# Performance work log

Hardware: AMD Instinct MI355X
Metric: run time of the kernel (lower is better)

## Reference

```python
import jax, jax.numpy as jnp
import numpy as np

B, DIN, DH, DOUT, E, GIN, GH = 16384, 480, 512, 360, 8, 64, 128


def setup_inputs() -> dict:
    key = jax.random.key(0)
    ks = jax.random.split(key, 16)

    def glorot(k, shape):
        bound = np.sqrt(6.0 / np.prod(shape[-2:]))
        return jax.random.uniform(k, shape, jnp.float32, -bound, bound)

    return {
        "x": jax.random.normal(ks[0], (B, DIN), jnp.float32),
        # norm stats: row0 = mean, row1 = std (kept away from 0)
        "Xnorm": jnp.stack([jax.random.normal(ks[1], (DIN,)) * 0.1,
                            jax.random.uniform(ks[2], (DIN,), minval=0.5, maxval=1.5)]),
        "Ynorm": jnp.stack([jax.random.normal(ks[3], (DOUT,)) * 0.1,
                            jax.random.uniform(ks[4], (DOUT,), minval=0.5, maxval=1.5)]),
        "G1_W": glorot(ks[5], (GIN, GH)), "G1_b": jnp.zeros((GH,), jnp.float32),
        "G2_W": glorot(ks[6], (GH, GH)), "G2_b": jnp.zeros((GH,), jnp.float32),
        "G3_W": glorot(ks[7], (GH, E)),  "G3_b": jnp.zeros((E,), jnp.float32),
        "W1": glorot(ks[8], (E, DIN, DH)), "b1": jnp.zeros((E, DH), jnp.float32),
        "W2": glorot(ks[9], (E, DH, DH)),  "b2": jnp.zeros((E, DH), jnp.float32),
        "W3": glorot(ks[10], (E, DH, DOUT)), "b3": jnp.zeros((E, DOUT), jnp.float32),
        "gating_indices": jnp.arange(GIN, dtype=jnp.int32),
    }


def expert_linear(h, w, W, b):
    # h: [B, I], w: [B, E], W: [E, I, O], b: [E, O]
    # sum_e w[:,e] * (h @ W[e] + b[e])
    y = jnp.einsum('bi,eio->beo', h, W)        # [B, E, O]
    return jnp.einsum('be,beo->bo', w, y) + w @ b


def reference(x, Xnorm, Ynorm, G1_W, G1_b, G2_W, G2_b, G3_W, G3_b,
              W1, b1, W2, b2, W3, b3, gating_indices):
    xn = (x - Xnorm[0]) / Xnorm[1]
    # gating network (dropout inactive at eval)
    g = xn[:, gating_indices]
    g = jax.nn.elu(g @ G1_W + G1_b)
    g = jax.nn.elu(g @ G2_W + G2_b)
    w = jax.nn.softmax(g @ G3_W + G3_b, axis=1)   # [B, E]
    # expert-blended main network
    m = jax.nn.elu(expert_linear(xn, w, W1, b1))
    m = jax.nn.elu(expert_linear(m, w, W2, b2))
    m = expert_linear(m, w, W3, b3)
    return m * Ynorm[1] + Ynorm[0]
```

## Files before the change

kernel.cpp:

```cpp
#include <hip/hip_runtime.h>
#include <hip/hip_bf16.h>
#include <math.h>

#define BATCH 16384
#define DIN   480
#define DH    512
#define DOUT  360
#define NEXP  8
#define GIN   64
#define GH    128
#define KP    512

typedef short bf16x8 __attribute__((ext_vector_type(8)));
typedef float f32x4  __attribute__((ext_vector_type(4)));

__device__ __forceinline__ short f2bf(float f) {
    __hip_bfloat16 h = __float2bfloat16(f);
    return *reinterpret_cast<short*>(&h);
}
__device__ __forceinline__ float eluf(float x) { return x > 0.f ? x : expf(x) - 1.f; }

__device__ __forceinline__ void gll16(const void* g, void* l) {
    __builtin_amdgcn_global_load_lds(
        (const __attribute__((address_space(1))) unsigned int*)g,
        (__attribute__((address_space(3))) unsigned int*)l, 16, 0, 0);
}

__global__ void prep_xn_kernel(const float* __restrict__ x,
                               const float* __restrict__ Xnorm,
                               short* __restrict__ xnbf) {
    const int tid = blockIdx.x * 256 + threadIdx.x;
    const int row = tid >> 6;
    const int c   = (tid & 63) * 8;
    short v8[8];
    if (c < DIN) {
        #pragma unroll
        for (int j = 0; j < 8; ++j) {
            float v = (x[(size_t)row * DIN + c + j] - Xnorm[c + j]) / Xnorm[DIN + c + j];
            v8[j] = f2bf(v);
        }
    } else {
        #pragma unroll
        for (int j = 0; j < 8; ++j) v8[j] = 0;
    }
    *(uint4*)&xnbf[(size_t)row * KP + c] = *(uint4*)v8;
}

__global__ void transpose_w_kernel(const float* __restrict__ src,
                                   short* __restrict__ dst,
                                   int K, int N, int NPAD) {
    __shared__ float tile[32][33];
    const int ntn = NPAD / 32;
    const int ntk = KP / 32;
    int lin = blockIdx.x;
    const int e  = lin / (ntk * ntn);
    lin -= e * ntk * ntn;
    const int kt = lin / ntn;
    const int nt = lin % ntn;
    const int t = threadIdx.x;
    #pragma unroll
    for (int r = 0; r < 4; ++r) {
        int idx = t + r * 256;
        int i = idx >> 5;
        int j = idx & 31;
        int k = kt * 32 + i;
        int n = nt * 32 + j;
        float v = (n < N && k < K) ? src[((size_t)e * K + k) * N + n] : 0.f;
        tile[i][j] = v;
    }
    __syncthreads();
    #pragma unroll
    for (int r = 0; r < 4; ++r) {
        int idx = t + r * 256;
        int i2 = idx & 31;
        int j2 = idx >> 5;
        dst[((size_t)e * NPAD + nt * 32 + j2) * KP + kt * 32 + i2] = f2bf(tile[i2][j2]);
    }
}

__global__ __launch_bounds__(256) void gating_kernel(
    const float* __restrict__ x, const float* __restrict__ Xnorm,
    const float* __restrict__ G1W, const float* __restrict__ G1b,
    const float* __restrict__ G2W, const float* __restrict__ G2b,
    const float* __restrict__ G3W, const float* __restrict__ G3b,
    const int* __restrict__ gidx, float* __restrict__ wout) {

    __shared__ float g2s[GH * GH];
    __shared__ float g3s[GH * NEXP];
    __shared__ float b1s[GH], b2s[GH], b3s[NEXP];
    __shared__ float g0b[4][GIN], h1b[4][GH], h2b[4][GH];

    const int t = threadIdx.x;
    const int lane = t & 63;
    const int wid  = t >> 6;

    for (int i = t; i < GH * GH; i += 256) g2s[i] = G2W[i];
    for (int i = t; i < GH * NEXP; i += 256) g3s[i] = G3W[i];
    if (t < GH) { b1s[t] = G1b[t]; b2s[t] = G2b[t]; }
    if (t < NEXP) b3s[t] = G3b[t];
    __syncthreads();

    const int gi = gidx[lane];
    const float mu = Xnorm[gi];
    const float inv_sig = 1.f / Xnorm[DIN + gi];

    for (int it = 0; it < 16; ++it) {
        const int row = (blockIdx.x * 4 + wid) * 16 + it;
        float g0 = (x[(size_t)row * DIN + gi] - mu) * inv_sig;
        g0b[wid][lane] = g0;
        __syncthreads();
        float h1a = b1s[lane], h1c = b1s[lane + 64];
        #pragma unroll 8
        for (int i = 0; i < GIN; ++i) {
            float g = g0b[wid][i];
            h1a += g * G1W[i * GH + lane];
            h1c += g * G1W[i * GH + lane + 64];
        }
        h1b[wid][lane] = eluf(h1a);
        h1b[wid][lane + 64] = eluf(h1c);
        __syncthreads();
        float h2a = b2s[lane], h2c = b2s[lane + 64];
        #pragma unroll 8
        for (int i = 0; i < GH; ++i) {
            float h = h1b[wid][i];
            h2a += h * g2s[i * GH + lane];
            h2c += h * g2s[i * GH + lane + 64];
        }
        h2b[wid][lane] = eluf(h2a);
        h2b[wid][lane + 64] = eluf(h2c);
        __syncthreads();
        const int e  = lane & 7;
        const int ch = lane >> 3;
        float p = 0.f;
        #pragma unroll
        for (int i2 = 0; i2 < 16; ++i2) {
            int i = ch * 16 + i2;
            p += h2b[wid][i] * g3s[i * NEXP + e];
        }
        p += __shfl_xor(p, 8);
        p += __shfl_xor(p, 16);
        p += __shfl_xor(p, 32);
        p += b3s[e];
        float mx = p;
        mx = fmaxf(mx, __shfl_xor(mx, 1));
        mx = fmaxf(mx, __shfl_xor(mx, 2));
        mx = fmaxf(mx, __shfl_xor(mx, 4));
        float ex = expf(p - mx);
        float sm = ex;
        sm += __shfl_xor(sm, 1);
        sm += __shfl_xor(sm, 2);
        sm += __shfl_xor(sm, 4);
        float wv = ex / sm;
        if (lane < NEXP) wout[(size_t)row * NEXP + lane] = wv;
        __syncthreads();
    }
}

template<int NPAD, int NREAL, int MODE>
__global__ __launch_bounds__(256, 2) void expert_v4_kernel(
    const short* __restrict__ A, const short* __restrict__ Wt,
    const float* __restrict__ wgate, const float* __restrict__ bias,
    const float* __restrict__ Ynorm, void* __restrict__ Out) {

    __shared__ __align__(16) short bufA[2][128 * 64];
    __shared__ __align__(16) short bufB[2][128 * 64];
    __shared__ float wlsT[NEXP][128];

    const int t = threadIdx.x;
    const int lane = t & 63;
    const int wid  = t >> 6;
    const int wr = wid >> 1, wc = wid & 1;
    const int l4 = lane >> 4, lr = lane & 15;

    constexpr int NN = NPAD / 128;
    const int nwg = 128 * NN;
    const int cpx = nwg >> 3;
    const int lb  = (blockIdx.x & 7) * cpx + (blockIdx.x >> 3);
    const int m0  = (lb / NN) * 128;
    const int n0  = (lb % NN) * 128;

    for (int i = t; i < NEXP * 128; i += 256) {
        int e = i >> 7, r = i & 127;
        wlsT[e][r] = wgate[(size_t)(m0 + r) * NEXP + e];
    }

    const int srow  = lane >> 3;
    const int sslot = (lane & 7) ^ srow;

    const short* baseA[4];
    const short* baseB[4];
    short* dstA[2][4];
    short* dstB[2][4];
    #pragma unroll
    for (int i = 0; i < 4; ++i) {
        int q = wid * 4 + i;
        baseA[i] = A  + (size_t)(m0 + q * 8 + srow) * KP + sslot * 8;
        baseB[i] = Wt + (size_t)(n0 + q * 8 + srow) * KP + sslot * 8;
        #pragma unroll
        for (int d = 0; d < 2; ++d) {
            dstA[d][i] = &bufA[d][q * 512];
            dstB[d][i] = &bufB[d][q * 512];
        }
    }

    f32x4 acc[4][4], accF[4][4];
    #pragma unroll
    for (int mi = 0; mi < 4; ++mi)
        #pragma unroll
        for (int ni = 0; ni < 4; ++ni) {
            acc[mi][ni]  = (f32x4){0.f, 0.f, 0.f, 0.f};
            accF[mi][ni] = (f32x4){0.f, 0.f, 0.f, 0.f};
        }

    #pragma unroll
    for (int i = 0; i < 4; ++i) {
        gll16(baseA[i], dstA[0][i]);
        gll16(baseB[i], dstB[0][i]);
    }
    __syncthreads();

    for (int s = 0; s < 8 * NEXP; ++s) {
        const int cur = s & 1;

        if (s < 8 * NEXP - 1) {
            const int sn  = s + 1;
            const int en  = sn >> 3;
            const int ktn = sn & 7;
            const size_t oa = (size_t)ktn * 64;
            const size_t ob = (size_t)en * NPAD * KP + (size_t)ktn * 64;
            #pragma unroll
            for (int i = 0; i < 4; ++i) gll16(baseA[i] + oa, dstA[cur ^ 1][i]);
            #pragma unroll
            for (int i = 0; i < 4; ++i) gll16(baseB[i] + ob, dstB[cur ^ 1][i]);
            asm volatile("s_waitcnt vmcnt(8)" ::: "memory");
        } else {
            asm volatile("s_waitcnt vmcnt(0)" ::: "memory");
        }
        asm volatile("s_barrier" ::: "memory");

        {
            const short* Ab = &bufA[cur][0];
            const short* Bb = &bufB[cur][0];
            #pragma unroll
            for (int kk = 0; kk < 2; ++kk) {
                const int xo = (kk * 32 + l4 * 8) ^ ((lr & 7) << 3);
                bf16x8 a[4], b[4];
                #pragma unroll
                for (int mi = 0; mi < 4; ++mi)
                    a[mi] = *(const bf16x8*)(Ab + (wr * 64 + mi * 16 + lr) * 64 + xo);
                #pragma unroll
                for (int ni = 0; ni < 4; ++ni)
                    b[ni] = *(const bf16x8*)(Bb + (wc * 64 + ni * 16 + lr) * 64 + xo);
                #pragma unroll
                for (int mi = 0; mi < 4; ++mi)
                    #pragma unroll
                    for (int ni = 0; ni < 4; ++ni)
                        acc[mi][ni] = __builtin_amdgcn_mfma_f32_16x16x32_bf16(
                            a[mi], b[ni], acc[mi][ni], 0, 0, 0);
            }
        }

        if ((s & 7) == 7) {
            const int e = s >> 3;
            #pragma unroll
            for (int mi = 0; mi < 4; ++mi) {
                f32x4 wv = *(const f32x4*)&wlsT[e][wr * 64 + mi * 16 + l4 * 4];
                #pragma unroll
                for (int ni = 0; ni < 4; ++ni) {
                    #pragma unroll
                    for (int j = 0; j < 4; ++j)
                        accF[mi][ni][j] += wv[j] * acc[mi][ni][j];
                    acc[mi][ni] = (f32x4){0.f, 0.f, 0.f, 0.f};
                }
            }
        }

        asm volatile("s_barrier" ::: "memory");
    }

    {
        float bv[4][NEXP];
        #pragma unroll
        for (int ni = 0; ni < 4; ++ni) {
            int ng = n0 + wc * 64 + ni * 16 + lr;
            #pragma unroll
            for (int e = 0; e < NEXP; ++e)
                bv[ni][e] = (ng < NREAL) ? bias[(size_t)e * NREAL + ng] : 0.f;
        }
        #pragma unroll
        for (int mi = 0; mi < 4; ++mi) {
            f32x4 wv[NEXP];
            #pragma unroll
            for (int e = 0; e < NEXP; ++e)
                wv[e] = *(const f32x4*)&wlsT[e][wr * 64 + mi * 16 + l4 * 4];
            #pragma unroll
            for (int ni = 0; ni < 4; ++ni)
                #pragma unroll
                for (int j = 0; j < 4; ++j) {
                    float sum = 0.f;
                    #pragma unroll
                    for (int e = 0; e < NEXP; ++e) sum += wv[e][j] * bv[ni][e];
                    accF[mi][ni][j] += sum;
                }
        }
    }

    #pragma unroll
    for (int mi = 0; mi < 4; ++mi) {
        #pragma unroll
        for (int j = 0; j < 4; ++j) {
            size_t rg = (size_t)(m0 + wr * 64 + mi * 16 + l4 * 4 + j);
            #pragma unroll
            for (int ni = 0; ni < 4; ++ni) {
                int ng = n0 + wc * 64 + ni * 16 + lr;
                float v = accF[mi][ni][j];
                if (MODE == 0) {
                    v = v > 0.f ? v : expf(v) - 1.f;
                    ((short*)Out)[rg * NPAD + ng] = f2bf(v);
                } else {
                    if (ng < NREAL)
                        ((float*)Out)[rg * NREAL + ng] = v * Ynorm[NREAL + ng] + Ynorm[ng];
                }
            }
        }
    }
}

extern "C" void kernel_launch(void* const* d_in, const int* in_sizes, int n_in,
                              void* d_out, int out_size, void* d_ws, size_t ws_size,
                              hipStream_t stream) {
    const float* x     = (const float*)d_in[0];
    const float* Xnorm = (const float*)d_in[1];
    const float* Ynorm = (const float*)d_in[2];
    const float* G1W   = (const float*)d_in[3];
    const float* G1b   = (const float*)d_in[4];
    const float* G2W   = (const float*)d_in[5];
    const float* G2b   = (const float*)d_in[6];
    const float* G3W   = (const float*)d_in[7];
    const float* G3b   = (const float*)d_in[8];
    const float* W1    = (const float*)d_in[9];
    const float* b1    = (const float*)d_in[10];
    const float* W2    = (const float*)d_in[11];
    const float* b2    = (const float*)d_in[12];
    const float* W3    = (const float*)d_in[13];
    const float* b3    = (const float*)d_in[14];
    const int*   gidx  = (const int*)d_in[15];

    char* ws = (char*)d_ws;
    size_t off = 0;
    short* xnbf = (short*)(ws + off); off += (size_t)BATCH * KP * 2;
    short* m1   = (short*)(ws + off); off += (size_t)BATCH * DH * 2;
    short* Wt1  = (short*)(ws + off); off += (size_t)NEXP * DH  * KP * 2;
    short* Wt2  = (short*)(ws + off); off += (size_t)NEXP * DH  * KP * 2;
    short* Wt3  = (short*)(ws + off); off += (size_t)NEXP * 384 * KP * 2;
    float* wg   = (float*)(ws + off); off += (size_t)BATCH * NEXP * 4;
    short* m2   = xnbf;
    if (off > ws_size) return;

    prep_xn_kernel<<<BATCH * 64 / 256, 256, 0, stream>>>(x, Xnorm, xnbf);

    transpose_w_kernel<<<NEXP * (KP / 32) * (DH / 32), 256, 0, stream>>>(W1, Wt1, DIN, DH, DH);
    transpose_w_kernel<<<NEXP * (KP / 32) * (DH / 32), 256, 0, stream>>>(W2, Wt2, DH, DH, DH);
    transpose_w_kernel<<<NEXP * (KP / 32) * (384 / 32), 256, 0, stream>>>(W3, Wt3, DH, DOUT, 384);

    gating_kernel<<<256, 256, 0, stream>>>(x, Xnorm, G1W, G1b, G2W, G2b, G3W, G3b, gidx, wg);

    expert_v4_kernel<DH, DH, 0>
        <<<(BATCH / 128) * (DH / 128), 256, 0, stream>>>(xnbf, Wt1, wg, b1, Ynorm, m1);
    expert_v4_kernel<DH, DH, 0>
        <<<(BATCH / 128) * (DH / 128), 256, 0, stream>>>(m1, Wt2, wg, b2, Ynorm, m2);
    expert_v4_kernel<384, DOUT, 1>
        <<<(BATCH / 128) * (384 / 128), 256, 0, stream>>>(m2, Wt3, wg, b3, Ynorm, (void*)d_out);
}
```

Baseline: 338.9 us.

## Restructure expert GEMM to load all experts per K-tile and reuse A fragments

```diff
diff --git a/kernel.cpp b/kernel.cpp
--- a/kernel.cpp
+++ b/kernel.cpp
@@ -157,149 +157,160 @@
 }
 
 template<int NPAD, int NREAL, int MODE>
-__global__ __launch_bounds__(256, 2) void expert_v4_kernel(
+__global__ __launch_bounds__(512, 1) void expert_v13_kernel(
     const short* __restrict__ A, const short* __restrict__ Wt,
     const float* __restrict__ wgate, const float* __restrict__ bias,
     const float* __restrict__ Ynorm, void* __restrict__ Out) {
 
-    __shared__ __align__(16) short bufA[2][128 * 64];
-    __shared__ __align__(16) short bufB[2][128 * 64];
-    __shared__ float wlsT[NEXP][128];
+    __shared__ __align__(16) short bufA[128 * 64];
+    __shared__ __align__(16) short bufB[NEXP][128 * 64];
+    __shared__ float    wlsT[NEXP][128];
+    __shared__ unsigned wpk2[512];
 
     const int t = threadIdx.x;
     const int lane = t & 63;
     const int wid  = t >> 6;
-    const int wr = wid >> 1, wc = wid & 1;
+    const int wr = wid >> 2;
+    const int wc = wid & 3;
     const int l4 = lane >> 4, lr = lane & 15;
 
     constexpr int NN = NPAD / 128;
-    const int nwg = 128 * NN;
-    const int cpx = nwg >> 3;
+    constexpr int nwg = (BATCH / 128) * NN;
+    constexpr int cpx = nwg / 8;
     const int lb  = (blockIdx.x & 7) * cpx + (blockIdx.x >> 3);
     const int m0  = (lb / NN) * 128;
     const int n0  = (lb % NN) * 128;
 
-    for (int i = t; i < NEXP * 128; i += 256) {
+    for (int i = t; i < NEXP * 128; i += 512) {
         int e = i >> 7, r = i & 127;
         wlsT[e][r] = wgate[(size_t)(m0 + r) * NEXP + e];
     }
-
-    const int srow  = lane >> 3;
-    const int sslot = (lane & 7) ^ srow;
-
-    const short* baseA[4];
-    const short* baseB[4];
-    short* dstA[2][4];
-    short* dstB[2][4];
-    #pragma unroll
-    for (int i = 0; i < 4; ++i) {
-        int q = wid * 4 + i;
-        baseA[i] = A  + (size_t)(m0 + q * 8 + srow) * KP + sslot * 8;
-        baseB[i] = Wt + (size_t)(n0 + q * 8 + srow) * KP + sslot * 8;
-        #pragma unroll
-        for (int d = 0; d < 2; ++d) {
-            dstA[d][i] = &bufA[d][q * 512];
-            dstB[d][i] = &bufB[d][q * 512];
-        }
-    }
-
-    f32x4 acc[4][4], accF[4][4];
+    {
+        int e = t >> 6, wr_ = (t >> 5) & 1, l4_ = (t >> 3) & 3, q = t & 7;
+        int mi_ = q >> 1, p = q & 1;
+        int r = wr_ * 64 + mi_ * 16 + l4_ * 4 + p * 2;
+        unsigned short b0 = (unsigned short)f2bf(wgate[(size_t)(m0 + r) * NEXP + e]);
+        unsigned short b1 = (unsigned short)f2bf(wgate[(size_t)(m0 + r + 1) * NEXP + e]);
+        wpk2[t] = ((unsigned)b1 << 16) | b0;
+    }
+
+    const int c0 = wid * 128 + lane;
+    const int c1 = c0 + 64;
+    const int r0 = c0 >> 3, s0 = (c0 & 7) ^ (r0 & 7);
+    const int r1 = c1 >> 3, s1 = (c1 & 7) ^ (r1 & 7);
+
+    const short* srcA0 = A + (size_t)(m0 + r0) * KP + s0 * 8;
+    const short* srcA1 = A + (size_t)(m0 + r1) * KP + s1 * 8;
+    const short* srcB0 = Wt + (size_t)(n0 + r0) * KP + s0 * 8;
+    const short* srcB1 = Wt + (size_t)(n0 + r1) * KP + s1 * 8;
+    short* const dstA0 = &bufA[c0 * 8];
+    short* const dstA1 = &bufA[c1 * 8];
+
+    f32x4 acc[4][2], accF[4][2];
     #pragma unroll
     for (int mi = 0; mi < 4; ++mi)
         #pragma unroll
-        for (int ni = 0; ni < 4; ++ni) {
-            acc[mi][ni]  = (f32x4){0.f, 0.f, 0.f, 0.f};
+        for (int ni = 0; ni < 2; ++ni)
             accF[mi][ni] = (f32x4){0.f, 0.f, 0.f, 0.f};
-        }
-
-    #pragma unroll
-    for (int i = 0; i < 4; ++i) {
-        gll16(baseA[i], dstA[0][i]);
-        gll16(baseB[i], dstB[0][i]);
-    }
-    __syncthreads();
-
-    for (int s = 0; s < 8 * NEXP; ++s) {
-        const int cur = s & 1;
-
-        if (s < 8 * NEXP - 1) {
-            const int sn  = s + 1;
-            const int en  = sn >> 3;
-            const int ktn = sn & 7;
-            const size_t oa = (size_t)ktn * 64;
-            const size_t ob = (size_t)en * NPAD * KP + (size_t)ktn * 64;
-            #pragma unroll
-            for (int i = 0; i < 4; ++i) gll16(baseA[i] + oa, dstA[cur ^ 1][i]);
-            #pragma unroll
-            for (int i = 0; i < 4; ++i) gll16(baseB[i] + ob, dstB[cur ^ 1][i]);
-            asm volatile("s_waitcnt vmcnt(8)" ::: "memory");
-        } else {
-            asm volatile("s_waitcnt vmcnt(0)" ::: "memory");
-        }
+    const f32x4 zf = (f32x4){0.f, 0.f, 0.f, 0.f};
+
+    const int xo0 = (l4 * 8) ^ ((lr & 7) << 3);
+    const int xo1 = (32 + l4 * 8) ^ ((lr & 7) << 3);
+    const int arow = (wr * 64 + lr) * 64;
+    const int brow = (wc * 32 + lr) * 64;
+    const int wbase = ((0 * 2 + wr) * 4 + l4) * 8;
+
+    #pragma unroll 1
+    for (int kt = 0; kt < 8; ++kt) {
+        __syncthreads();
+
+        const size_t ko = (size_t)kt * 64;
+        gll16(srcA0 + ko, dstA0);
+        gll16(srcA1 + ko, dstA1);
+        #pragma unroll
+        for (int e = 0; e < NEXP; ++e) {
+            const size_t eo = (size_t)e * NPAD * KP + ko;
+            gll16(srcB0 + eo, &bufB[e][c0 * 8]);
+            gll16(srcB1 + eo, &bufB[e][c1 * 8]);
+        }
+        asm volatile("s_waitcnt vmcnt(0)" ::: "memory");
         asm volatile("s_barrier" ::: "memory");
 
-        {
-            const short* Ab = &bufA[cur][0];
-            const short* Bb = &bufB[cur][0];
-            #pragma unroll
-            for (int kk = 0; kk < 2; ++kk) {
-                const int xo = (kk * 32 + l4 * 8) ^ ((lr & 7) << 3);
-                bf16x8 a[4], b[4];
-                #pragma unroll
-                for (int mi = 0; mi < 4; ++mi)
-                    a[mi] = *(const bf16x8*)(Ab + (wr * 64 + mi * 16 + lr) * 64 + xo);
-                #pragma unroll
-                for (int ni = 0; ni < 4; ++ni)
-                    b[ni] = *(const bf16x8*)(Bb + (wc * 64 + ni * 16 + lr) * 64 + xo);
+        bf16x8 af0[4], af1[4];
+        #pragma unroll
+        for (int mi = 0; mi < 4; ++mi) {
+            af0[mi] = *(const bf16x8*)(&bufA[arow + mi * 1024 + xo0]);
+            af1[mi] = *(const bf16x8*)(&bufA[arow + mi * 1024 + xo1]);
+        }
+
+        #pragma unroll 1
+        for (int j = 0; j < 8; ++j) {
+            const int e_ = (wid + j) & 7;
+            const short* Bb = &bufB[e_][0];
+
+            bf16x8 b00, b01, b10, b11;
+            b00 = *(const bf16x8*)(Bb + brow + 0 * 1024 + xo0);
+            b01 = *(const bf16x8*)(Bb + brow + 1 * 1024 + xo0);
+            b10 = *(const bf16x8*)(Bb + brow + 0 * 1024 + xo1);
+            b11 = *(const bf16x8*)(Bb + brow + 1 * 1024 + xo1);
+
+            __builtin_amdgcn_s_setprio(1);
+            #pragma unroll
+            for (int mi = 0; mi < 4; ++mi) {
+                acc[mi][0] = __builtin_amdgcn_mfma_f32_16x16x32_bf16(af0[mi], b00, zf, 0, 0, 0);
+                acc[mi][1] = __builtin_amdgcn_mfma_f32_16x16x32_bf16(af0[mi], b01, zf, 0, 0, 0);
+            }
+            #pragma unroll
+            for (int mi = 0; mi < 4; ++mi) {
+                acc[mi][0] = __builtin_amdgcn_mfma_f32_16x16x32_bf16(af1[mi], b10, acc[mi][0], 0, 0, 0);
+                acc[mi][1] = __builtin_amdgcn_mfma_f32_16x16x32_bf16(af1[mi], b11, acc[mi][1], 0, 0, 0);
+            }
+            __builtin_amdgcn_s_setprio(0);
+
+            {
+                const int wb = wbase + e_ * 64;
+                uint4 uq0 = *(const uint4*)&wpk2[wb];
+                uint4 uq1 = *(const uint4*)&wpk2[wb + 4];
+                unsigned uu[8] = {uq0.x, uq0.y, uq0.z, uq0.w,
+                                  uq1.x, uq1.y, uq1.z, uq1.w};
                 #pragma unroll
                 for (int mi = 0; mi < 4; ++mi)
                     #pragma unroll
-                    for (int ni = 0; ni < 4; ++ni)
-                        acc[mi][ni] = __builtin_amdgcn_mfma_f32_16x16x32_bf16(
-                            a[mi], b[ni], acc[mi][ni], 0, 0, 0);
+                    for (int p = 0; p < 2; ++p) {
+                        const unsigned u = uu[mi * 2 + p];
+                        const float w0 = __uint_as_float(u << 16);
+                        const float w1 = __uint_as_float(u & 0xffff0000u);
+                        accF[mi][0][p * 2]     += w0 * acc[mi][0][p * 2];
+                        accF[mi][1][p * 2]     += w0 * acc[mi][1][p * 2];
+                        accF[mi][0][p * 2 + 1] += w1 * acc[mi][0][p * 2 + 1];
+                        accF[mi][1][p * 2 + 1] += w1 * acc[mi][1][p * 2 + 1];
+                    }
             }
         }
-
-        if ((s & 7) == 7) {
-            const int e = s >> 3;
-            #pragma unroll
-            for (int mi = 0; mi < 4; ++mi) {
-                f32x4 wv = *(const f32x4*)&wlsT[e][wr * 64 + mi * 16 + l4 * 4];
-                #pragma unroll
-                for (int ni = 0; ni < 4; ++ni) {
-                    #pragma unroll
-                    for (int j = 0; j < 4; ++j)
-                        accF[mi][ni][j] += wv[j] * acc[mi][ni][j];
-                    acc[mi][ni] = (f32x4){0.f, 0.f, 0.f, 0.f};
-                }
-            }
-        }
-
-        asm volatile("s_barrier" ::: "memory");
     }
 
     {
-        float bv[4][NEXP];
-        #pragma unroll
-        for (int ni = 0; ni < 4; ++ni) {
-            int ng = n0 + wc * 64 + ni * 16 + lr;
+        float bv[2][NEXP];
+        #pragma unroll
+        for (int ni = 0; ni < 2; ++ni) {
+            int ng = n0 + wc * 32 + ni * 16 + lr;
             #pragma unroll
             for (int e = 0; e < NEXP; ++e)
                 bv[ni][e] = (ng < NREAL) ? bias[(size_t)e * NREAL + ng] : 0.f;
         }
         #pragma unroll
         for (int mi = 0; mi < 4; ++mi) {
-            f32x4 wv[NEXP];
+            f32x4 wve[NEXP];
             #pragma unroll
             for (int e = 0; e < NEXP; ++e)
-                wv[e] = *(const f32x4*)&wlsT[e][wr * 64 + mi * 16 + l4 * 4];
-            #pragma unroll
-            for (int ni = 0; ni < 4; ++ni)
+                wve[e] = *(const f32x4*)&wlsT[e][wr * 64 + mi * 16 + l4 * 4];
+            #pragma unroll
+            for (int ni = 0; ni < 2; ++ni)
                 #pragma unroll
                 for (int j = 0; j < 4; ++j) {
                     float sum = 0.f;
                     #pragma unroll
-                    for (int e = 0; e < NEXP; ++e) sum += wv[e][j] * bv[ni][e];
+                    for (int e = 0; e < NEXP; ++e) sum += wve[e][j] * bv[ni][e];
                     accF[mi][ni][j] += sum;
                 }
         }
@@ -311,8 +322,8 @@
         for (int j = 0; j < 4; ++j) {
             size_t rg = (size_t)(m0 + wr * 64 + mi * 16 + l4 * 4 + j);
             #pragma unroll
-            for (int ni = 0; ni < 4; ++ni) {
-                int ng = n0 + wc * 64 + ni * 16 + lr;
+            for (int ni = 0; ni < 2; ++ni) {
+                int ng = n0 + wc * 32 + ni * 16 + lr;
                 float v = accF[mi][ni][j];
                 if (MODE == 0) {
                     v = v > 0.f ? v : expf(v) - 1.f;
@@ -365,10 +376,10 @@
 
     gating_kernel<<<256, 256, 0, stream>>>(x, Xnorm, G1W, G1b, G2W, G2b, G3W, G3b, gidx, wg);
 
-    expert_v4_kernel<DH, DH, 0>
-        <<<(BATCH / 128) * (DH / 128), 256, 0, stream>>>(xnbf, Wt1, wg, b1, Ynorm, m1);
-    expert_v4_kernel<DH, DH, 0>
-        <<<(BATCH / 128) * (DH / 128), 256, 0, stream>>>(m1, Wt2, wg, b2, Ynorm, m2);
-    expert_v4_kernel<384, DOUT, 1>
-        <<<(BATCH / 128) * (384 / 128), 256, 0, stream>>>(m2, Wt3, wg, b3, Ynorm, (void*)d_out);
-}
+    expert_v13_kernel<DH, DH, 0>
+        <<<(BATCH / 128) * (DH / 128), 512, 0, stream>>>(xnbf, Wt1, wg, b1, Ynorm, m1);
+    expert_v13_kernel<DH, DH, 0>
+        <<<(BATCH / 128) * (DH / 128), 512, 0, stream>>>(m1, Wt2, wg, b2, Ynorm, m2);
+    expert_v13_kernel<384, DOUT, 1>
+        <<<(BATCH / 128) * (384 / 128), 512, 0, stream>>>(m2, Wt3, wg, b3, Ynorm, (void*)d_out);
+}
```

Result: slower. 404.7 us (+19.4%).
